# Kernel tuning notes

Hardware: AMD Instinct MI355X
Metric: run time of the kernel (lower is better)

The kernel has to match this reference:

```python
import jax, jax.numpy as jnp
import numpy as np
import math

N_QUBITS = 8
N_QLAYERS = 1
LN_EPS = 1e-5


def _rx(state, theta, wire, n):
    # state: (N, 2,...,2) complex64 with n qubit axes; theta: (N,)
    sh = (theta.shape[0],) + (1,) * (n - 1)
    c = jnp.cos(theta / 2).reshape(sh)
    s = jnp.sin(theta / 2).reshape(sh)
    a = jax.lax.index_in_dim(state, 0, wire + 1, keepdims=False)
    b = jax.lax.index_in_dim(state, 1, wire + 1, keepdims=False)
    return jnp.stack([c * a - 1j * s * b, -1j * s * a + c * b], axis=wire + 1)


def _cnot(state, cw, tw, n):
    s0 = jax.lax.index_in_dim(state, 0, cw + 1, keepdims=False)
    s1 = jax.lax.index_in_dim(state, 1, cw + 1, keepdims=False)
    t_ax = tw + 1 if tw < cw else tw  # target axis index after removing control axis
    s1 = jnp.flip(s1, axis=t_ax)
    return jnp.stack([s0, s1], axis=cw + 1)


def _quantum(angles, qweights):
    # AngleEmbedding (RX) + BasicEntanglerLayers (RX + CNOT ring) + PauliZ expvals
    # angles: (N, 8) float; qweights: (1, 8) float -> returns (N, 8) float
    n = N_QUBITS
    N = angles.shape[0]
    state = jnp.zeros((N,) + (2,) * n, jnp.complex64)
    state = state.at[(slice(None),) + (0,) * n].set(1.0 + 0j)
    for w in range(n):
        state = _rx(state, angles[:, w], w, n)
    for l in range(N_QLAYERS):
        for w in range(n):
            state = _rx(state, jnp.broadcast_to(qweights[l, w], (N,)), w, n)
        for cw in range(n):
            state = _cnot(state, cw, (cw + 1) % n, n)
    probs = state.real ** 2 + state.imag ** 2
    zs = []
    for w in range(n):
        p = probs.sum(axis=tuple(a for a in range(1, n + 1) if a != w + 1))  # (N, 2)
        zs.append(p[:, 0] - p[:, 1])
    return jnp.stack(zs, axis=-1)


def _layernorm(x, g, b):
    m = x.mean(-1, keepdims=True)
    v = ((x - m) ** 2).mean(-1, keepdims=True)
    return (x - m) / jnp.sqrt(v + LN_EPS) * g + b


def _forward(x, Wq, Wk, Wv, Wo, ln1_g, ln1_b, W1, b1, W2, b2, ln2_g, ln2_b,
             ql1_w, ql1_b, qweights, ql2_w, ql2_b):
    B, S, D = x.shape
    H = 16
    dk = D // H
    q = (x @ Wq.T).reshape(B, S, H, dk)
    k = (x @ Wk.T).reshape(B, S, H, dk)
    v = (x @ Wv.T).reshape(B, S, H, dk)
    scores = jnp.einsum('bqhd,bkhd->bhqk', q, k) * (1.0 / math.sqrt(dk))
    attn = jax.nn.softmax(scores, axis=-1)
    o = jnp.einsum('bhqk,bkhd->bqhd', attn, v).reshape(B, S, D) @ Wo.T
    x = _layernorm(o + x, ln1_g, ln1_b)
    ff = jax.nn.relu(x @ W1.T + b1) @ W2.T + b2
    x = _layernorm(ff + x, ln2_g, ln2_b)
    angles = (x @ ql1_w.T + ql1_b).reshape(B * S, N_QUBITS)
    z = _quantum(angles, qweights).reshape(B, S, N_QUBITS).astype(x.dtype)
    y = jnp.concatenate([z, x], axis=2) @ ql2_w.T + ql2_b
    return y


def setup_inputs() -> dict:
    key = jax.random.key(0)
    ks = jax.random.split(key, 12)
    B, S, D, F = 4, 1024, 1024, 4096
    sc = 0.02
    w = lambda k, *sh: jax.random.normal(k, sh, jnp.float32) * sc
    return {
        'x': jax.random.normal(ks[0], (B, S, D), jnp.float32),
        'Wq': w(ks[1], D, D), 'Wk': w(ks[2], D, D), 'Wv': w(ks[3], D, D), 'Wo': w(ks[4], D, D),
        'ln1_g': jnp.ones((D,), jnp.float32), 'ln1_b': jnp.zeros((D,), jnp.float32),
        'W1': w(ks[5], F, D), 'b1': jnp.zeros((F,), jnp.float32),
        'W2': w(ks[6], D, F), 'b2': jnp.zeros((D,), jnp.float32),
        'ln2_g': jnp.ones((D,), jnp.float32), 'ln2_b': jnp.zeros((D,), jnp.float32),
        'ql1_w': w(ks[7], N_QUBITS, D), 'ql1_b': jnp.zeros((N_QUBITS,), jnp.float32),
        'qweights': jax.random.uniform(ks[8], (N_QLAYERS, N_QUBITS), jnp.float32, 0.0, 2 * np.pi),
        'ql2_w': w(ks[9], D, D + N_QUBITS), 'ql2_b': jnp.zeros((D,), jnp.float32),
    }


def reference(x, Wq, Wk, Wv, Wo, ln1_g, ln1_b, W1, b1, W2, b2, ln2_g, ln2_b,
              ql1_w, ql1_b, qweights, ql2_w, ql2_b):
    return _forward(x, Wq, Wk, Wv, Wo, ln1_g, ln1_b, W1, b1, W2, b2, ln2_g, ln2_b,
                    ql1_w, ql1_b, qweights, ql2_w, ql2_b)
```

## Files before the change

kernel.cpp:

```cpp
#include <hip/hip_runtime.h>
#include <hip/hip_bf16.h>

typedef __bf16 bf16_t;
typedef __attribute__((ext_vector_type(8))) __bf16 bf16x8;
typedef __attribute__((ext_vector_type(4))) float floatx4;

#define BM 128

enum { EPI_NONE = 0, EPI_RESID, EPI_BIAS_RELU, EPI_BIAS_RESID, EPI_QL2, EPI_PART };

__device__ __forceinline__ void gld_lds16(const bf16_t* g, bf16_t* l) {
  __builtin_amdgcn_global_load_lds(
      (__attribute__((address_space(1))) void*)(g),
      (__attribute__((address_space(3))) void*)(l), 16, 0, 0);
}

template<int ROWS, int COLS>
__device__ __forceinline__ void stage_swz(const bf16_t* g, int ld, bf16_t* lds, int tid) {
  constexpr int G = COLS / 8;
  #pragma unroll
  for (int i = 0; i < ROWS * G / 256; ++i) {
    int ci = i * 256 + tid;
    int row = ci / G, cc = ci % G;
    int gg = (G == 8) ? (cc ^ (row & 7)) : ((cc & 8) | ((cc & 7) ^ (row & 7)));
    gld_lds16(g + (size_t)row * ld + gg * 8, lds + ci * 8);
  }
}

__device__ __forceinline__ int xcd_remap(int id, int nwg) {
  return (id & 7) * (nwg >> 3) + (id >> 3);
}

__device__ __forceinline__ void core128(const bf16_t* __restrict__ Ag,
                                        const bf16_t* __restrict__ Bg,
                                        int Kloop, int lda, int ldb,
                                        bf16_t* As, bf16_t* Bs,
                                        floatx4 acc[4][4]) {
  const int tid = threadIdx.x;
  const int wid = tid >> 6, lane = tid & 63;
  const int wm = (wid >> 1) * 64, wn = (wid & 1) * 64;
  const int m16 = lane & 15, quad = lane >> 4;
  const int r7 = m16 & 7;
  constexpr int BUF = BM * 64;
  const int NT = Kloop >> 6;
  stage_swz<128, 64>(Ag, lda, As, tid);
  stage_swz<128, 64>(Bg, ldb, Bs, tid);
  if (NT > 1) {
    stage_swz<128, 64>(Ag + 64, lda, As + BUF, tid);
    stage_swz<128, 64>(Bg + 64, ldb, Bs + BUF, tid);
    asm volatile("s_waitcnt vmcnt(8)" ::: "memory");
  } else {
    asm volatile("s_waitcnt vmcnt(0)" ::: "memory");
  }
  asm volatile("s_barrier" ::: "memory");
  for (int t = 0; t < NT; ++t) {
    const bf16_t* Ab = As + (t & 1) * BUF;
    const bf16_t* Bb = Bs + (t & 1) * BUF;
    #pragma unroll
    for (int ks = 0; ks < 2; ++ks) {
      const int gi = ks * 4 + quad;
      const int slot = gi ^ r7;
      bf16x8 af[4], bfr[4];
      #pragma unroll
      for (int mt = 0; mt < 4; ++mt)
        af[mt] = *(const bf16x8*)&Ab[((wm + mt * 16 + m16) * 8 + slot) * 8];
      #pragma unroll
      for (int nt = 0; nt < 4; ++nt)
        bfr[nt] = *(const bf16x8*)&Bb[((wn + nt * 16 + m16) * 8 + slot) * 8];
      #pragma unroll
      for (int mt = 0; mt < 4; ++mt)
        #pragma unroll
        for (int nt = 0; nt < 4; ++nt)
          acc[mt][nt] = __builtin_amdgcn_mfma_f32_16x16x32_bf16(af[mt], bfr[nt], acc[mt][nt], 0, 0, 0);
    }
    if (t + 1 < NT) {
      asm volatile("s_waitcnt lgkmcnt(0)" ::: "memory");
      asm volatile("s_barrier" ::: "memory");
      if (t + 2 < NT) {
        stage_swz<128, 64>(Ag + (t + 2) * 64, lda, As + (t & 1) * BUF, tid);
        stage_swz<128, 64>(Bg + (t + 2) * 64, ldb, Bs + (t & 1) * BUF, tid);
        asm volatile("s_waitcnt vmcnt(8)" ::: "memory");
      } else {
        asm volatile("s_waitcnt vmcnt(0)" ::: "memory");
      }
      asm volatile("s_barrier" ::: "memory");
    }
  }
}

template<int EPI>
__global__ __launch_bounds__(256)
void gemm128(const bf16_t* __restrict__ A, const bf16_t* __restrict__ B,
             bf16_t* __restrict__ C, const float* __restrict__ bias,
             int N, int K, int mblocks, int nblocks) {
  __shared__ bf16_t As[2 * BM * 64];
  __shared__ bf16_t Bs[2 * BM * 64];
  const int tid = threadIdx.x;
  const int wid = tid >> 6, lane = tid & 63;
  const int wm = (wid >> 1) * 64, wn = (wid & 1) * 64;
  const int m16 = lane & 15, quad = lane >> 4;
  const int id = xcd_remap(blockIdx.x, gridDim.x);
  const int per_group = 8 * nblocks;
  const int grp = id / per_group, rem = id % per_group;
  const int m0 = (grp * 8 + (rem & 7)) * BM;
  const int n0 = (rem >> 3) * BM;
  floatx4 acc[4][4];
  const floatx4 vzero = {0.f, 0.f, 0.f, 0.f};
  #pragma unroll
  for (int mt = 0; mt < 4; ++mt)
    #pragma unroll
    for (int nt = 0; nt < 4; ++nt) acc[mt][nt] = vzero;
  core128(A + (size_t)m0 * K, B + (size_t)n0 * K, K, K, K, As, Bs, acc);
  #pragma unroll
  for (int mt = 0; mt < 4; ++mt)
    #pragma unroll
    for (int nt = 0; nt < 4; ++nt) {
      const int gcol = n0 + wn + nt * 16 + m16;
      float bv = (EPI == EPI_BIAS_RELU) ? bias[gcol] : 0.f;
      #pragma unroll
      for (int r = 0; r < 4; ++r) {
        const int grow = m0 + wm + mt * 16 + quad * 4 + r;
        float v = acc[mt][nt][r];
        if (EPI == EPI_BIAS_RELU) { v += bv; v = fmaxf(v, 0.f); }
        C[(size_t)grow * N + gcol] = (bf16_t)v;
      }
    }
}

__global__ __launch_bounds__(256)
void gemm128_sk(const bf16_t* __restrict__ A, const bf16_t* __restrict__ B,
                bf16_t* __restrict__ p0, bf16_t* __restrict__ p1,
                int N, int K, int ldb, int mblocks, int nblocks) {
  __shared__ bf16_t As[2 * BM * 64];
  __shared__ bf16_t Bs[2 * BM * 64];
  const int tid = threadIdx.x;
  const int wid = tid >> 6, lane = tid & 63;
  const int wm = (wid >> 1) * 64, wn = (wid & 1) * 64;
  const int m16 = lane & 15, quad = lane >> 4;
  const int id = xcd_remap(blockIdx.x, gridDim.x);
  const int per_kh = mblocks * nblocks;
  const int kh = id / per_kh;
  const int rem2 = id % per_kh;
  const int per_group = 8 * nblocks;
  const int grp = rem2 / per_group, rem = rem2 % per_group;
  const int m0 = (grp * 8 + (rem & 7)) * BM;
  const int n0 = (rem >> 3) * BM;
  const int Keff = K / 2;
  floatx4 acc[4][4];
  const floatx4 vzero = {0.f, 0.f, 0.f, 0.f};
  #pragma unroll
  for (int mt = 0; mt < 4; ++mt)
    #pragma unroll
    for (int nt = 0; nt < 4; ++nt) acc[mt][nt] = vzero;
  core128(A + (size_t)m0 * K + (size_t)kh * Keff,
          B + (size_t)n0 * ldb + (size_t)kh * Keff, Keff, K, ldb, As, Bs, acc);
  bf16_t* Cp = kh ? p1 : p0;
  #pragma unroll
  for (int mt = 0; mt < 4; ++mt)
    #pragma unroll
    for (int nt = 0; nt < 4; ++nt) {
      const int gcol = n0 + wn + nt * 16 + m16;
      #pragma unroll
      for (int r = 0; r < 4; ++r) {
        const int grow = m0 + wm + mt * 16 + quad * 4 + r;
        Cp[(size_t)grow * N + gcol] = (bf16_t)acc[mt][nt][r];
      }
    }
}

__global__ __launch_bounds__(256)
void gemm_qkv(const bf16_t* __restrict__ X, const bf16_t* __restrict__ Wb,
              bf16_t* __restrict__ Qo, bf16_t* __restrict__ Ko, bf16_t* __restrict__ Vt) {
  __shared__ bf16_t As[2 * BM * 64];
  __shared__ bf16_t Bs[2 * BM * 64];
  const int tid = threadIdx.x;
  const int wid = tid >> 6, lane = tid & 63;
  const int wm = (wid >> 1) * 64, wn = (wid & 1) * 64;
  const int m16 = lane & 15, quad = lane >> 4;
  const int id = xcd_remap(blockIdx.x, gridDim.x);
  const int per_group = 8 * 24;
  const int grp = id / per_group, rem = id % per_group;
  const int m0 = (grp * 8 + (rem & 7)) * BM;
  const int nall = rem >> 3;
  const int n0 = (nall & 7) * BM;
  const int sel = nall >> 3;
  const bf16_t* B = Wb + (size_t)sel * 1024 * 1024;
  floatx4 acc[4][4];
  const floatx4 vzero = {0.f, 0.f, 0.f, 0.f};
  #pragma unroll
  for (int mt = 0; mt < 4; ++mt)
    #pragma unroll
    for (int nt = 0; nt < 4; ++nt) acc[mt][nt] = vzero;
  core128(X + (size_t)m0 * 1024, B + (size_t)n0 * 1024, 1024, 1024, 1024, As, Bs, acc);
  if (sel < 2) {
    bf16_t* C = sel ? Ko : Qo;
    const float sc = sel ? 1.f : 0.125f;
    #pragma unroll
    for (int mt = 0; mt < 4; ++mt)
      #pragma unroll
      for (int nt = 0; nt < 4; ++nt) {
        const int gcol = n0 + wn + nt * 16 + m16;
        #pragma unroll
        for (int r = 0; r < 4; ++r) {
          const int grow = m0 + wm + mt * 16 + quad * 4 + r;
          C[(size_t)grow * 1024 + gcol] = (bf16_t)(acc[mt][nt][r] * sc);
        }
      }
  } else {
    #pragma unroll
    for (int mt = 0; mt < 4; ++mt) {
      const int grow0 = m0 + wm + mt * 16 + quad * 4;
      const int b = grow0 >> 10, s = grow0 & 1023;
      #pragma unroll
      for (int nt = 0; nt < 4; ++nt) {
        const int gcol = n0 + wn + nt * 16 + m16;
        const int h = gcol >> 6, d = gcol & 63;
        #pragma unroll
        for (int r = 0; r < 4; ++r)
          Vt[(((size_t)b * 16 + h) * 64 + d) * 1024 + s + r] = (bf16_t)acc[mt][nt][r];
      }
    }
  }
}

template<int EPI, bool OUTF32>
__global__ __launch_bounds__(256)
void gemm64(const bf16_t* __restrict__ A, const bf16_t* __restrict__ B,
            void* __restrict__ Cv,
            const bf16_t* __restrict__ resid, const float* __restrict__ bias,
            const bf16_t* __restrict__ z, const float* __restrict__ zw,
            int N, int K, int ldb, int boff, int mblocks) {
  __shared__ bf16_t As[BM * 128];
  __shared__ bf16_t Bs[64 * 128];
  const int tid = threadIdx.x;
  const int wid = tid >> 6, lane = tid & 63;
  const int wm = (wid >> 1) * 64, wn = (wid & 1) * 32;
  const int m16 = lane & 15, quad = lane >> 4;
  const int r7 = m16 & 7;
  const int id = xcd_remap(blockIdx.x, gridDim.x);
  const int nb_ = N >> 6;
  const int per_group = 8 * nb_;
  const int grp = id / per_group, rem = id % per_group;
  const int m0 = (grp * 8 + (rem & 7)) * BM;
  const int n0 = (rem >> 3) * 64;
  const bf16_t* Ag = A + (size_t)m0 * K;
  const bf16_t* Bg = B + (size_t)n0 * ldb + boff;
  floatx4 acc[4][2];
  const floatx4 vzero = {0.f, 0.f, 0.f, 0.f};
  #pragma unroll
  for (int mt = 0; mt < 4; ++mt)
    #pragma unroll
    for (int nt = 0; nt < 2; ++nt) acc[mt][nt] = vzero;
  for (int k0 = 0; k0 < K; k0 += 128) {
    stage_swz<128, 128>(Ag + k0, K, As, tid);
    stage_swz<64, 128>(Bg + k0, ldb, Bs, tid);
    __syncthreads();
    #pragma unroll
    for (int ks = 0; ks < 4; ++ks) {
      const int gi = ks * 4 + quad;
      const int slot = (gi & 8) | ((gi & 7) ^ r7);
      bf16x8 af[4], bfr[2];
      #pragma unroll
      for (int mt = 0; mt < 4; ++mt)
        af[mt] = *(const bf16x8*)&As[((wm + mt * 16 + m16) * 16 + slot) * 8];
      #pragma unroll
      for (int nt = 0; nt < 2; ++nt)
        bfr[nt] = *(const bf16x8*)&Bs[((wn + nt * 16 + m16) * 16 + slot) * 8];
      #pragma unroll
      for (int mt = 0; mt < 4; ++mt)
        #pragma unroll
        for (int nt = 0; nt < 2; ++nt)
          acc[mt][nt] = __builtin_amdgcn_mfma_f32_16x16x32_bf16(af[mt], bfr[nt], acc[mt][nt], 0, 0, 0);
    }
    __syncthreads();
  }
  #pragma unroll
  for (int mt = 0; mt < 4; ++mt)
    #pragma unroll
    for (int nt = 0; nt < 2; ++nt) {
      const int gcol = n0 + wn + nt * 16 + m16;
      float bv = 0.f;
      if (EPI == EPI_QL2) bv = bias[gcol];
      #pragma unroll
      for (int r = 0; r < 4; ++r) {
        const int grow = m0 + wm + mt * 16 + quad * 4 + r;
        float v = acc[mt][nt][r];
        if (EPI == EPI_RESID) v += (float)resid[(size_t)grow * N + gcol];
        if (EPI == EPI_QL2) {
          float s = 0.f;
          #pragma unroll
          for (int u = 0; u < 8; ++u)
            s += (float)z[(size_t)grow * 8 + u] * zw[(size_t)gcol * 1032 + u];
          v += bv + s;
        }
        if (OUTF32) ((float*)Cv)[(size_t)grow * N + gcol] = v;
        else        ((bf16_t*)Cv)[(size_t)grow * N + gcol] = (bf16_t)v;
      }
    }
}

__global__ __launch_bounds__(256)
void attn_kernel(const bf16_t* __restrict__ Q, const bf16_t* __restrict__ Kb,
                 const bf16_t* __restrict__ Vt, bf16_t* __restrict__ O) {
  __shared__ bf16_t Qs[64 * 64];
  __shared__ bf16_t Ks[2][128 * 64];
  __shared__ bf16_t Vs[64 * 128];
  __shared__ bf16_t Ps[4][16 * 128];
  const int tid = threadIdx.x;
  const int wid = tid >> 6, lane = tid & 63;
  const int m16 = lane & 15, quad = lane >> 4;
  const int id = blockIdx.x;
  const int bh = (id & 7) * 8 + ((id >> 3) & 7);
  const int qt = id >> 6;
  const int b = bh >> 4, h = bh & 15;
  const size_t qbase = ((size_t)(b * 1024 + qt * 64)) * 1024 + h * 64;
  const size_t kbase = ((size_t)(b * 1024)) * 1024 + h * 64;
  const size_t vbase = ((size_t)bh * 64) * 1024;
  #pragma unroll
  for (int i = 0; i < 2; ++i) {
    int ci = i * 256 + tid;
    int row = ci >> 3, cc = ci & 7;
    *(bf16x8*)&Qs[row * 64 + ((cc ^ (row & 7)) * 8)] =
        *(const bf16x8*)&Q[qbase + (size_t)row * 1024 + cc * 8];
  }
  stage_swz<128, 64>(Kb + kbase, 1024, Ks[0], tid);
  asm volatile("s_waitcnt vmcnt(0)" ::: "memory");
  __syncthreads();
  const int qm = wid * 16 + m16;
  bf16x8 qf0 = *(const bf16x8*)&Qs[qm * 64 + ((quad ^ (qm & 7)) * 8)];
  bf16x8 qf1 = *(const bf16x8*)&Qs[qm * 64 + (((4 + quad) ^ (qm & 7)) * 8)];
  floatx4 oacc[4];
  float rs[4];
  const floatx4 vzero = {0.f, 0.f, 0.f, 0.f};
  #pragma unroll
  for (int dt = 0; dt < 4; ++dt) oacc[dt] = vzero;
  #pragma unroll
  for (int r = 0; r < 4; ++r) rs[r] = 0.f;
  for (int kt = 0; kt < 8; ++kt) {
    stage_swz<64, 128>(Vt + vbase + kt * 128, 1024, Vs, tid);
    if (kt < 7)
      stage_swz<128, 64>(Kb + kbase + (size_t)(kt + 1) * 128 * 1024, 1024, Ks[(kt + 1) & 1], tid);
    const bf16_t* Kc = Ks[kt & 1];
    floatx4 sa[8];
    #pragma unroll
    for (int nt = 0; nt < 8; ++nt) sa[nt] = vzero;
    #pragma unroll
    for (int nt = 0; nt < 8; ++nt) {
      const int n = nt * 16 + m16;
      bf16x8 kf0 = *(const bf16x8*)&Kc[n * 64 + ((quad ^ (n & 7)) * 8)];
      bf16x8 kf1 = *(const bf16x8*)&Kc[n * 64 + (((4 + quad) ^ (n & 7)) * 8)];
      sa[nt] = __builtin_amdgcn_mfma_f32_16x16x32_bf16(qf0, kf0, sa[nt], 0, 0, 0);
      sa[nt] = __builtin_amdgcn_mfma_f32_16x16x32_bf16(qf1, kf1, sa[nt], 0, 0, 0);
    }
    #pragma unroll
    for (int nt = 0; nt < 8; ++nt)
      #pragma unroll
      for (int r = 0; r < 4; ++r) {
        float pv = __expf(sa[nt][r]);
        rs[r] += pv;
        const int prow = quad * 4 + r;
        const int g = nt * 2 + (m16 >> 3);
        const int gs = (g & 8) | ((g & 7) ^ (prow & 7));
        Ps[wid][prow * 128 + gs * 8 + (m16 & 7)] = (bf16_t)pv;
      }
    asm volatile("s_waitcnt vmcnt(0)" ::: "memory");
    __syncthreads();
    bf16x8 pf[4];
    #pragma unroll
    for (int ksub = 0; ksub < 4; ++ksub) {
      const int g = ksub * 4 + quad;
      const int gs = (g & 8) | ((g & 7) ^ (m16 & 7));
      pf[ksub] = *(const bf16x8*)&Ps[wid][m16 * 128 + gs * 8];
    }
    #pragma unroll
    for (int dt = 0; dt < 4; ++dt) {
      const int n = dt * 16 + m16;
      #pragma unroll
      for (int ksub = 0; ksub < 4; ++ksub) {
        const int g = ksub * 4 + quad;
        const int gs = (g & 8) | ((g & 7) ^ (n & 7));
        bf16x8 vf = *(const bf16x8*)&Vs[n * 128 + gs * 8];
        oacc[dt] = __builtin_amdgcn_mfma_f32_16x16x32_bf16(pf[ksub], vf, oacc[dt], 0, 0, 0);
      }
    }
    __syncthreads();
  }
  #pragma unroll
  for (int r = 0; r < 4; ++r) {
    rs[r] += __shfl_xor(rs[r], 1);
    rs[r] += __shfl_xor(rs[r], 2);
    rs[r] += __shfl_xor(rs[r], 4);
    rs[r] += __shfl_xor(rs[r], 8);
  }
  const size_t obase = ((size_t)(b * 1024 + qt * 64 + wid * 16)) * 1024 + h * 64;
  #pragma unroll
  for (int dt = 0; dt < 4; ++dt)
    #pragma unroll
    for (int r = 0; r < 4; ++r)
      O[obase + (size_t)(quad * 4 + r) * 1024 + dt * 16 + m16] = (bf16_t)(oacc[dt][r] / rs[r]);
}

struct Segs {
  const float* s[5];
  bf16_t* d[5];
  int n8[5];
};
__global__ __launch_bounds__(256)
void conv_multi(Segs sg) {
  const int zz = blockIdx.z;
  const float* in = sg.s[zz];
  bf16_t* out = sg.d[zz];
  const int n8 = sg.n8[zz];
  for (int i = blockIdx.x * 256 + threadIdx.x; i < n8; i += gridDim.x * 256) {
    const float* p = in + (size_t)i * 8;
    floatx4 a = *(const floatx4*)p;
    floatx4 b = *(const floatx4*)(p + 4);
    bf16x8 o;
    #pragma unroll
    for (int j = 0; j < 4; ++j) { o[j] = (bf16_t)a[j]; o[4 + j] = (bf16_t)b[j]; }
    *(bf16x8*)(out + (size_t)i * 8) = o;
  }
}

__global__ __launch_bounds__(256)
void ln_combine(const bf16_t* __restrict__ p0, const bf16_t* __restrict__ p1,
                const bf16_t* __restrict__ resid,
                const float* __restrict__ g, const float* __restrict__ b,
                bf16_t* __restrict__ out) {
  const int row = blockIdx.x * 4 + (threadIdx.x >> 6);
  const int lane = threadIdx.x & 63;
  const size_t base = (size_t)row * 1024 + lane * 16;
  bf16x8 a0 = *(const bf16x8*)&p0[base];
  bf16x8 a1 = *(const bf16x8*)&p0[base + 8];
  bf16x8 b0 = *(const bf16x8*)&p1[base];
  bf16x8 b1 = *(const bf16x8*)&p1[base + 8];
  bf16x8 c0 = *(const bf16x8*)&resid[base];
  bf16x8 c1 = *(const bf16x8*)&resid[base + 8];
  float f[16];
  #pragma unroll
  for (int j = 0; j < 8; ++j) {
    f[j]     = (float)a0[j] + (float)b0[j] + (float)c0[j];
    f[8 + j] = (float)a1[j] + (float)b1[j] + (float)c1[j];
  }
  float s = 0.f, ss = 0.f;
  #pragma unroll
  for (int j = 0; j < 16; ++j) { s += f[j]; ss += f[j] * f[j]; }
  #pragma unroll
  for (int off = 1; off < 64; off <<= 1) { s += __shfl_xor(s, off); ss += __shfl_xor(ss, off); }
  const float m = s * (1.f / 1024.f);
  const float inv_sd = rsqrtf(ss * (1.f / 1024.f) - m * m + 1e-5f);
  const float* gp = g + lane * 16;
  const float* bp = b + lane * 16;
  bf16x8 o0, o1;
  #pragma unroll
  for (int j = 0; j < 8; ++j) o0[j] = (bf16_t)((f[j] - m) * inv_sd * gp[j] + bp[j]);
  #pragma unroll
  for (int j = 0; j < 8; ++j) o1[j] = (bf16_t)((f[8 + j] - m) * inv_sd * gp[8 + j] + bp[8 + j]);
  *(bf16x8*)&out[base] = o0;
  *(bf16x8*)&out[base + 8] = o1;
}

__global__ __launch_bounds__(256)
void ln2_quantum(const bf16_t* __restrict__ p0, const bf16_t* __restrict__ p1,
                 const bf16_t* __restrict__ resid, const float* __restrict__ bias,
                 const float* __restrict__ g, const float* __restrict__ b,
                 bf16_t* __restrict__ x2,
                 const float* __restrict__ qw1, const float* __restrict__ qb1,
                 const float* __restrict__ qwt, bf16_t* __restrict__ zout,
                 const float* __restrict__ ql2w, bf16_t* __restrict__ ql2wb) {
  if (blockIdx.z == 1) {
    const int n8 = 1024 * 1032 / 8;
    for (int i = blockIdx.x * 256 + threadIdx.x; i < n8; i += gridDim.x * 256) {
      const float* p = ql2w + (size_t)i * 8;
      floatx4 a = *(const floatx4*)p;
      floatx4 bb = *(const floatx4*)(p + 4);
      bf16x8 o;
      #pragma unroll
      for (int j = 0; j < 4; ++j) { o[j] = (bf16_t)a[j]; o[4 + j] = (bf16_t)bb[j]; }
      *(bf16x8*)(ql2wb + (size_t)i * 8) = o;
    }
    return;
  }
  const int row = blockIdx.x * 4 + (threadIdx.x >> 6);
  const int lane = threadIdx.x & 63;
  const size_t base = (size_t)row * 1024 + lane * 16;
  bf16x8 a0 = *(const bf16x8*)&p0[base];
  bf16x8 a1 = *(const bf16x8*)&p0[base + 8];
  bf16x8 b0 = *(const bf16x8*)&p1[base];
  bf16x8 b1 = *(const bf16x8*)&p1[base + 8];
  bf16x8 c0 = *(const bf16x8*)&resid[base];
  bf16x8 c1 = *(const bf16x8*)&resid[base + 8];
  const float* bsp = bias + lane * 16;
  float f[16];
  #pragma unroll
  for (int j = 0; j < 8; ++j) {
    f[j]     = (float)a0[j] + (float)b0[j] + (float)c0[j] + bsp[j];
    f[8 + j] = (float)a1[j] + (float)b1[j] + (float)c1[j] + bsp[8 + j];
  }
  float s = 0.f, ss = 0.f;
  #pragma unroll
  for (int j = 0; j < 16; ++j) { s += f[j]; ss += f[j] * f[j]; }
  #pragma unroll
  for (int off = 1; off < 64; off <<= 1) { s += __shfl_xor(s, off); ss += __shfl_xor(ss, off); }
  const float m = s * (1.f / 1024.f);
  const float inv_sd = rsqrtf(ss * (1.f / 1024.f) - m * m + 1e-5f);
  const float* gp = g + lane * 16;
  const float* bp = b + lane * 16;
  bf16x8 o0, o1;
  #pragma unroll
  for (int j = 0; j < 8; ++j) o0[j] = (bf16_t)((f[j] - m) * inv_sd * gp[j] + bp[j]);
  #pragma unroll
  for (int j = 0; j < 8; ++j) o1[j] = (bf16_t)((f[8 + j] - m) * inv_sd * gp[8 + j] + bp[8 + j]);
  *(bf16x8*)&x2[base] = o0;
  *(bf16x8*)&x2[base + 8] = o1;
  float th[8];
  #pragma unroll
  for (int qq = 0; qq < 8; ++qq) {
    const float* wp = qw1 + (size_t)qq * 1024 + lane * 16;
    float sdot = 0.f;
    #pragma unroll
    for (int j = 0; j < 8; ++j)
      sdot += (float)o0[j] * wp[j] + (float)o1[j] * wp[8 + j];
    #pragma unroll
    for (int off = 1; off < 64; off <<= 1) sdot += __shfl_xor(sdot, off);
    th[qq] = sdot + qb1[qq] + qwt[qq];
  }
  if (lane == 0) {
    float c[8];
    #pragma unroll
    for (int qq = 0; qq < 8; ++qq) c[qq] = cosf(th[qq]);
    float z0 = 1.f;
    #pragma unroll
    for (int u = 1; u < 8; ++u) z0 *= c[u];
    zout[(size_t)row * 8 + 0] = (bf16_t)z0;
    float pp = c[0];
    #pragma unroll
    for (int w = 1; w < 8; ++w) { pp *= c[w]; zout[(size_t)row * 8 + w] = (bf16_t)pp; }
  }
}

extern "C" void kernel_launch(void* const* d_in, const int* in_sizes, int n_in,
                              void* d_out, int out_size, void* d_ws, size_t ws_size,
                              hipStream_t stream) {
  const float* x    = (const float*)d_in[0];
  const float* Wq   = (const float*)d_in[1];
  const float* Wk   = (const float*)d_in[2];
  const float* Wv   = (const float*)d_in[3];
  const float* Wo   = (const float*)d_in[4];
  const float* ln1g = (const float*)d_in[5];
  const float* ln1b = (const float*)d_in[6];
  const float* W1   = (const float*)d_in[7];
  const float* b1   = (const float*)d_in[8];
  const float* W2   = (const float*)d_in[9];
  const float* b2   = (const float*)d_in[10];
  const float* ln2g = (const float*)d_in[11];
  const float* ln2b = (const float*)d_in[12];
  const float* qw1  = (const float*)d_in[13];
  const float* qb1  = (const float*)d_in[14];
  const float* qwt  = (const float*)d_in[15];
  const float* ql2w = (const float*)d_in[16];
  const float* ql2b = (const float*)d_in[17];
  bf16_t* ws = (bf16_t*)d_ws;

  const size_t T = (size_t)4096 * 1024;
  const size_t M1 = (size_t)1024 * 1024;
  bf16_t* outlo = (bf16_t*)d_out;
  bf16_t* outhi = outlo + T;

  bf16_t* xb    = ws;
  bf16_t* kb    = ws + T;
  bf16_t* vt    = ws + 2 * T;
  bf16_t* ff    = ws + 3 * T;
  bf16_t* wqkvb = ff;
  bf16_t* wob   = ff + 3 * M1;
  bf16_t* w1b   = vt;
  bf16_t* w2b   = kb;
  bf16_t* ql2wb = ff;
  bf16_t* q     = outlo;
  bf16_t* o     = outhi;
  bf16_t* x1    = outhi;
  bf16_t* x2    = vt;
  bf16_t* z     = kb;

  {
    Segs sg;
    sg.s[0] = x;  sg.d[0] = xb;            sg.n8[0] = (int)(T / 8);
    sg.s[1] = Wq; sg.d[1] = wqkvb;         sg.n8[1] = (int)(M1 / 8);
    sg.s[2] = Wk; sg.d[2] = wqkvb + M1;    sg.n8[2] = (int)(M1 / 8);
    sg.s[3] = Wv; sg.d[3] = wqkvb + 2*M1;  sg.n8[3] = (int)(M1 / 8);
    sg.s[4] = Wo; sg.d[4] = wob;           sg.n8[4] = (int)(M1 / 8);
    conv_multi<<<dim3(512, 1, 5), 256, 0, stream>>>(sg);
  }
  gemm_qkv<<<768, 256, 0, stream>>>(xb, wqkvb, q, kb, vt);
  attn_kernel<<<1024, 256, 0, stream>>>(q, kb, vt, o);
  gemm128_sk<<<512, 256, 0, stream>>>(o, wob, outlo, kb, 1024, 1024, 1024, 32, 8);
  ln_combine<<<1024, 256, 0, stream>>>(outlo, kb, xb, ln1g, ln1b, x1);
  {
    Segs sg;
    sg.s[0] = W1; sg.d[0] = w1b; sg.n8[0] = (int)(T / 8);
    sg.s[1] = W2; sg.d[1] = w2b; sg.n8[1] = (int)(T / 8);
    sg.s[2] = nullptr; sg.d[2] = nullptr; sg.n8[2] = 0;
    sg.s[3] = nullptr; sg.d[3] = nullptr; sg.n8[3] = 0;
    sg.s[4] = nullptr; sg.d[4] = nullptr; sg.n8[4] = 0;
    conv_multi<<<dim3(1024, 1, 2), 256, 0, stream>>>(sg);
  }
  gemm128<EPI_BIAS_RELU><<<1024, 256, 0, stream>>>(x1, w1b, ff, b1, 4096, 1024, 32, 32);
  gemm128_sk<<<512, 256, 0, stream>>>(ff, w2b, xb, vt, 1024, 4096, 4096, 32, 8);
  ln2_quantum<<<dim3(1024, 1, 2), 256, 0, stream>>>(
      xb, vt, x1, b2, ln2g, ln2b, x2, qw1, qb1, qwt, z, ql2w, ql2wb);
  gemm64<EPI_QL2, true><<<512, 256, 0, stream>>>(
      x2, ql2wb, d_out, nullptr, ql2b, z, ql2w, 1024, 1024, 1032, 8, 32);
}
```

Before: 377.9 us.

## Enlarge GEMM tiles to 256x128 with 8 waves and triple-buffered LDS pipeline

```diff
diff --git a/kernel.cpp b/kernel.cpp
--- a/kernel.cpp
+++ b/kernel.cpp
@@ -15,12 +15,12 @@
       (__attribute__((address_space(3))) void*)(l), 16, 0, 0);
 }
 
-template<int ROWS, int COLS>
+template<int ROWS, int COLS, int NTHR>
 __device__ __forceinline__ void stage_swz(const bf16_t* g, int ld, bf16_t* lds, int tid) {
   constexpr int G = COLS / 8;
   #pragma unroll
-  for (int i = 0; i < ROWS * G / 256; ++i) {
-    int ci = i * 256 + tid;
+  for (int i = 0; i < ROWS * G / NTHR; ++i) {
+    int ci = i * NTHR + tid;
     int row = ci / G, cc = ci % G;
     int gg = (G == 8) ? (cc ^ (row & 7)) : ((cc & 8) | ((cc & 7) ^ (row & 7)));
     gld_lds16(g + (size_t)row * ld + gg * 8, lds + ci * 8);
@@ -31,31 +31,38 @@
   return (id & 7) * (nwg >> 3) + (id >> 3);
 }
 
-__device__ __forceinline__ void core128(const bf16_t* __restrict__ Ag,
+__device__ __forceinline__ void core256(const bf16_t* __restrict__ Ag,
                                         const bf16_t* __restrict__ Bg,
                                         int Kloop, int lda, int ldb,
                                         bf16_t* As, bf16_t* Bs,
                                         floatx4 acc[4][4]) {
   const int tid = threadIdx.x;
   const int wid = tid >> 6, lane = tid & 63;
-  const int wm = (wid >> 1) * 64, wn = (wid & 1) * 64;
+  const int wm = (wid >> 1) * 64;
+  const int wn = (wid & 1) * 64;
   const int m16 = lane & 15, quad = lane >> 4;
   const int r7 = m16 & 7;
-  constexpr int BUF = BM * 64;
+  constexpr int ABUF = 256 * 64, BBUF = 128 * 64;
   const int NT = Kloop >> 6;
-  stage_swz<128, 64>(Ag, lda, As, tid);
-  stage_swz<128, 64>(Bg, ldb, Bs, tid);
+  stage_swz<256, 64, 512>(Ag, lda, As, tid);
+  stage_swz<128, 64, 512>(Bg, ldb, Bs, tid);
   if (NT > 1) {
-    stage_swz<128, 64>(Ag + 64, lda, As + BUF, tid);
-    stage_swz<128, 64>(Bg + 64, ldb, Bs + BUF, tid);
-    asm volatile("s_waitcnt vmcnt(8)" ::: "memory");
+    stage_swz<256, 64, 512>(Ag + 64, lda, As + ABUF, tid);
+    stage_swz<128, 64, 512>(Bg + 64, ldb, Bs + BBUF, tid);
+    asm volatile("s_waitcnt vmcnt(6)" ::: "memory");
   } else {
     asm volatile("s_waitcnt vmcnt(0)" ::: "memory");
   }
   asm volatile("s_barrier" ::: "memory");
+  int bsel = 0;
   for (int t = 0; t < NT; ++t) {
-    const bf16_t* Ab = As + (t & 1) * BUF;
-    const bf16_t* Bb = Bs + (t & 1) * BUF;
+    int nsel = bsel + 2; if (nsel >= 3) nsel -= 3;
+    if (t + 2 < NT) {
+      stage_swz<256, 64, 512>(Ag + (t + 2) * 64, lda, As + nsel * ABUF, tid);
+      stage_swz<128, 64, 512>(Bg + (t + 2) * 64, ldb, Bs + nsel * BBUF, tid);
+    }
+    const bf16_t* Ab = As + bsel * ABUF;
+    const bf16_t* Bb = Bs + bsel * BBUF;
     #pragma unroll
     for (int ks = 0; ks < 2; ++ks) {
       const int gi = ks * 4 + quad;
@@ -73,28 +80,24 @@
         for (int nt = 0; nt < 4; ++nt)
           acc[mt][nt] = __builtin_amdgcn_mfma_f32_16x16x32_bf16(af[mt], bfr[nt], acc[mt][nt], 0, 0, 0);
     }
-    if (t + 1 < NT) {
-      asm volatile("s_waitcnt lgkmcnt(0)" ::: "memory");
-      asm volatile("s_barrier" ::: "memory");
-      if (t + 2 < NT) {
-        stage_swz<128, 64>(Ag + (t + 2) * 64, lda, As + (t & 1) * BUF, tid);
-        stage_swz<128, 64>(Bg + (t + 2) * 64, ldb, Bs + (t & 1) * BUF, tid);
-        asm volatile("s_waitcnt vmcnt(8)" ::: "memory");
-      } else {
-        asm volatile("s_waitcnt vmcnt(0)" ::: "memory");
-      }
-      asm volatile("s_barrier" ::: "memory");
-    }
+    asm volatile("s_waitcnt lgkmcnt(0)" ::: "memory");
+    if (t + 2 < NT) {
+      asm volatile("s_waitcnt vmcnt(6)" ::: "memory");
+    } else if (t + 1 < NT) {
+      asm volatile("s_waitcnt vmcnt(0)" ::: "memory");
+    }
+    if (t + 1 < NT) asm volatile("s_barrier" ::: "memory");
+    bsel += 1; if (bsel == 3) bsel = 0;
   }
 }
 
 template<int EPI>
-__global__ __launch_bounds__(256)
+__global__ __launch_bounds__(512)
 void gemm128(const bf16_t* __restrict__ A, const bf16_t* __restrict__ B,
              bf16_t* __restrict__ C, const float* __restrict__ bias,
              int N, int K, int mblocks, int nblocks) {
-  __shared__ bf16_t As[2 * BM * 64];
-  __shared__ bf16_t Bs[2 * BM * 64];
+  __shared__ bf16_t As[3 * 256 * 64];
+  __shared__ bf16_t Bs[3 * 128 * 64];
   const int tid = threadIdx.x;
   const int wid = tid >> 6, lane = tid & 63;
   const int wm = (wid >> 1) * 64, wn = (wid & 1) * 64;
@@ -102,15 +105,15 @@
   const int id = xcd_remap(blockIdx.x, gridDim.x);
   const int per_group = 8 * nblocks;
   const int grp = id / per_group, rem = id % per_group;
-  const int m0 = (grp * 8 + (rem & 7)) * BM;
-  const int n0 = (rem >> 3) * BM;
+  const int m0 = (grp * 8 + (rem & 7)) * 256;
+  const int n0 = (rem >> 3) * 128;
   floatx4 acc[4][4];
   const floatx4 vzero = {0.f, 0.f, 0.f, 0.f};
   #pragma unroll
   for (int mt = 0; mt < 4; ++mt)
     #pragma unroll
     for (int nt = 0; nt < 4; ++nt) acc[mt][nt] = vzero;
-  core128(A + (size_t)m0 * K, B + (size_t)n0 * K, K, K, K, As, Bs, acc);
+  core256(A + (size_t)m0 * K, B + (size_t)n0 * K, K, K, K, As, Bs, acc);
   #pragma unroll
   for (int mt = 0; mt < 4; ++mt)
     #pragma unroll
@@ -127,12 +130,12 @@
     }
 }
 
-__global__ __launch_bounds__(256)
+__global__ __launch_bounds__(512)
 void gemm128_sk(const bf16_t* __restrict__ A, const bf16_t* __restrict__ B,
                 bf16_t* __restrict__ p0, bf16_t* __restrict__ p1,
                 int N, int K, int ldb, int mblocks, int nblocks) {
-  __shared__ bf16_t As[2 * BM * 64];
-  __shared__ bf16_t Bs[2 * BM * 64];
+  __shared__ bf16_t As[3 * 256 * 64];
+  __shared__ bf16_t Bs[3 * 128 * 64];
   const int tid = threadIdx.x;
   const int wid = tid >> 6, lane = tid & 63;
   const int wm = (wid >> 1) * 64, wn = (wid & 1) * 64;
@@ -143,8 +146,8 @@
   const int rem2 = id % per_kh;
   const int per_group = 8 * nblocks;
   const int grp = rem2 / per_group, rem = rem2 % per_group;
-  const int m0 = (grp * 8 + (rem & 7)) * BM;
-  const int n0 = (rem >> 3) * BM;
+  const int m0 = (grp * 8 + (rem & 7)) * 256;
+  const int n0 = (rem >> 3) * 128;
   const int Keff = K / 2;
   floatx4 acc[4][4];
   const floatx4 vzero = {0.f, 0.f, 0.f, 0.f};
@@ -152,7 +155,7 @@
   for (int mt = 0; mt < 4; ++mt)
     #pragma unroll
     for (int nt = 0; nt < 4; ++nt) acc[mt][nt] = vzero;
-  core128(A + (size_t)m0 * K + (size_t)kh * Keff,
+  core256(A + (size_t)m0 * K + (size_t)kh * Keff,
           B + (size_t)n0 * ldb + (size_t)kh * Keff, Keff, K, ldb, As, Bs, acc);
   bf16_t* Cp = kh ? p1 : p0;
   #pragma unroll
@@ -168,11 +171,11 @@
     }
 }
 
-__global__ __launch_bounds__(256)
+__global__ __launch_bounds__(512)
 void gemm_qkv(const bf16_t* __restrict__ X, const bf16_t* __restrict__ Wb,
               bf16_t* __restrict__ Qo, bf16_t* __restrict__ Ko, bf16_t* __restrict__ Vt) {
-  __shared__ bf16_t As[2 * BM * 64];
-  __shared__ bf16_t Bs[2 * BM * 64];
+  __shared__ bf16_t As[3 * 256 * 64];
+  __shared__ bf16_t Bs[3 * 128 * 64];
   const int tid = threadIdx.x;
   const int wid = tid >> 6, lane = tid & 63;
   const int wm = (wid >> 1) * 64, wn = (wid & 1) * 64;
@@ -180,9 +183,9 @@
   const int id = xcd_remap(blockIdx.x, gridDim.x);
   const int per_group = 8 * 24;
   const int grp = id / per_group, rem = id % per_group;
-  const int m0 = (grp * 8 + (rem & 7)) * BM;
+  const int m0 = (grp * 8 + (rem & 7)) * 256;
   const int nall = rem >> 3;
-  const int n0 = (nall & 7) * BM;
+  const int n0 = (nall & 7) * 128;
   const int sel = nall >> 3;
   const bf16_t* B = Wb + (size_t)sel * 1024 * 1024;
   floatx4 acc[4][4];
@@ -191,7 +194,7 @@
   for (int mt = 0; mt < 4; ++mt)
     #pragma unroll
     for (int nt = 0; nt < 4; ++nt) acc[mt][nt] = vzero;
-  core128(X + (size_t)m0 * 1024, B + (size_t)n0 * 1024, 1024, 1024, 1024, As, Bs, acc);
+  core256(X + (size_t)m0 * 1024, B + (size_t)n0 * 1024, 1024, 1024, 1024, As, Bs, acc);
   if (sel < 2) {
     bf16_t* C = sel ? Ko : Qo;
     const float sc = sel ? 1.f : 0.125f;
@@ -252,8 +255,8 @@
     #pragma unroll
     for (int nt = 0; nt < 2; ++nt) acc[mt][nt] = vzero;
   for (int k0 = 0; k0 < K; k0 += 128) {
-    stage_swz<128, 128>(Ag + k0, K, As, tid);
-    stage_swz<64, 128>(Bg + k0, ldb, Bs, tid);
+    stage_swz<128, 128, 256>(Ag + k0, K, As, tid);
+    stage_swz<64, 128, 256>(Bg + k0, ldb, Bs, tid);
     __syncthreads();
     #pragma unroll
     for (int ks = 0; ks < 4; ++ks) {
@@ -323,7 +326,7 @@
     *(bf16x8*)&Qs[row * 64 + ((cc ^ (row & 7)) * 8)] =
         *(const bf16x8*)&Q[qbase + (size_t)row * 1024 + cc * 8];
   }
-  stage_swz<128, 64>(Kb + kbase, 1024, Ks[0], tid);
+  stage_swz<128, 64, 256>(Kb + kbase, 1024, Ks[0], tid);
   asm volatile("s_waitcnt vmcnt(0)" ::: "memory");
   __syncthreads();
   const int qm = wid * 16 + m16;
@@ -337,9 +340,9 @@
   #pragma unroll
   for (int r = 0; r < 4; ++r) rs[r] = 0.f;
   for (int kt = 0; kt < 8; ++kt) {
-    stage_swz<64, 128>(Vt + vbase + kt * 128, 1024, Vs, tid);
+    stage_swz<64, 128, 256>(Vt + vbase + kt * 128, 1024, Vs, tid);
     if (kt < 7)
-      stage_swz<128, 64>(Kb + kbase + (size_t)(kt + 1) * 128 * 1024, 1024, Ks[(kt + 1) & 1], tid);
+      stage_swz<128, 64, 256>(Kb + kbase + (size_t)(kt + 1) * 128 * 1024, 1024, Ks[(kt + 1) & 1], tid);
     const bf16_t* Kc = Ks[kt & 1];
     floatx4 sa[8];
     #pragma unroll
@@ -591,9 +594,9 @@
     sg.s[4] = Wo; sg.d[4] = wob;           sg.n8[4] = (int)(M1 / 8);
     conv_multi<<<dim3(512, 1, 5), 256, 0, stream>>>(sg);
   }
-  gemm_qkv<<<768, 256, 0, stream>>>(xb, wqkvb, q, kb, vt);
+  gemm_qkv<<<384, 512, 0, stream>>>(xb, wqkvb, q, kb, vt);
   attn_kernel<<<1024, 256, 0, stream>>>(q, kb, vt, o);
-  gemm128_sk<<<512, 256, 0, stream>>>(o, wob, outlo, kb, 1024, 1024, 1024, 32, 8);
+  gemm128_sk<<<256, 512, 0, stream>>>(o, wob, outlo, kb, 1024, 1024, 1024, 16, 8);
   ln_combine<<<1024, 256, 0, stream>>>(outlo, kb, xb, ln1g, ln1b, x1);
   {
     Segs sg;
@@ -604,8 +607,8 @@
     sg.s[4] = nullptr; sg.d[4] = nullptr; sg.n8[4] = 0;
     conv_multi<<<dim3(1024, 1, 2), 256, 0, stream>>>(sg);
   }
-  gemm128<EPI_BIAS_RELU><<<1024, 256, 0, stream>>>(x1, w1b, ff, b1, 4096, 1024, 32, 32);
-  gemm128_sk<<<512, 256, 0, stream>>>(ff, w2b, xb, vt, 1024, 4096, 4096, 32, 8);
+  gemm128<EPI_BIAS_RELU><<<512, 512, 0, stream>>>(x1, w1b, ff, b1, 4096, 1024, 16, 32);
+  gemm128_sk<<<256, 512, 0, stream>>>(ff, w2b, xb, vt, 1024, 4096, 4096, 16, 8);
   ln2_quantum<<<dim3(1024, 1, 2), 256, 0, stream>>>(
       xb, vt, x1, b2, ln2g, ln2b, x2, qw1, qb1, qwt, z, ql2w, ql2wb);
   gemm64<EPI_QL2, true><<<512, 256, 0, stream>>>(
```

Result: slower. 403.9 us (+6.9%).
